# Kernel optimization log

Hardware: AMD Instinct MI355X
Metric: run time of the kernel (lower is better)

The kernel has to match this reference:

```python
import jax, jax.numpy as jnp
import numpy as np

B, T, F, U = 64, 256, 64, 512  # batch, bid_sequence, features, lstm units


def setup_inputs() -> dict:
    key = jax.random.key(0)
    ks = jax.random.split(key, 8)
    sc = 0.05
    return {
        "inputs": jax.random.normal(ks[0], (B, T, F), jnp.float32),
        "kernel": jax.random.normal(ks[1], (F, 4 * U), jnp.float32) * sc,      # LSTM input kernel (i,f,c,o)
        "rec_kernel": jax.random.normal(ks[2], (U, 4 * U), jnp.float32) * sc,  # LSTM recurrent kernel
        "bias": jax.random.normal(ks[3], (4 * U,), jnp.float32) * sc,          # LSTM bias
        "att_W": jax.random.normal(ks[4], (T, T), jnp.float32) * sc,           # row t = weights of attention_denses[t] (first t cols used)
        "att_b": jax.random.normal(ks[5], (T,), jnp.float32) * sc,             # bias of attention_denses[t]
        "out_W": jax.random.normal(ks[6], (U,), jnp.float32) * sc,             # final Dense(1) kernel
        "out_b": jax.random.normal(ks[7], (), jnp.float32) * sc,               # final Dense(1) bias
    }


def reference(inputs, kernel, rec_kernel, bias, att_W, att_b, out_W, out_b):
    Bs, Ts, _ = inputs.shape
    Us = rec_kernel.shape[0]

    # ---- LSTM (keras LSTMCell, gate order i,f,c,o; sigmoid/tanh) ----
    xz = jnp.einsum('btf,fg->btg', inputs, kernel) + bias  # precompute input projection

    def step(carry, z):
        h, c = carry
        g = z + h @ rec_kernel
        i, f, gc, o = jnp.split(g, 4, axis=-1)
        c = jax.nn.sigmoid(f) * c + jax.nn.sigmoid(i) * jnp.tanh(gc)
        h = jax.nn.sigmoid(o) * jnp.tanh(c)
        return (h, c), h

    init = (jnp.zeros((Bs, Us), inputs.dtype), jnp.zeros((Bs, Us), inputs.dtype))
    _, hs = jax.lax.scan(step, init, jnp.swapaxes(xz, 0, 1))
    x = jnp.swapaxes(hs, 0, 1)  # (B, T, U)

    # ---- attention_loop ----
    # keras Attention([x[:t], [x[t]]]) softmaxes over a single key -> weights are
    # exactly 1, so attn output is x[t] tiled t times; transpose + Dense_t(1)
    # collapses to sum(att_W[t, :t]) * x[t] + att_b[t]. Step 0 passes x[0] through.
    t_idx = jnp.arange(Ts)
    tri = (t_idx[None, :] < t_idx[:, None]).astype(x.dtype)  # row t: first t cols valid
    coef = jnp.where(t_idx == 0, jnp.asarray(1.0, x.dtype), jnp.sum(att_W * tri, axis=1))
    shift = jnp.where(t_idx == 0, jnp.asarray(0.0, x.dtype), att_b)
    att = x * coef[None, :, None] + shift[None, :, None]  # (B, T, U)

    # ---- final Dense(1) + reshape + sigmoid ----
    return jax.nn.sigmoid(jnp.einsum('btu,u->bt', att, out_W) + out_b)  # (B, T)
```

## Files before the change

kernel.cpp:

```cpp
#include <hip/hip_runtime.h>
#include <hip/hip_bf16.h>
#include <string.h>

#define B_ 64
#define T_ 256
#define F_ 64
#define U_ 512
#define G4_ 2048
#define KTOT 576
#define KSTEPS 18

typedef __attribute__((ext_vector_type(8))) short short8;
typedef __attribute__((ext_vector_type(4))) float v4f;
typedef __attribute__((ext_vector_type(4))) int i4;
typedef unsigned short u16;

__device__ __forceinline__ float bf2f(u16 b) {
    unsigned int x = ((unsigned int)b) << 16;
    float f; memcpy(&f, &x, 4); return f;
}
__device__ __forceinline__ u16 f2bf(float f) {
    __hip_bfloat16 h = __float2bfloat16(f);
    u16 b; memcpy(&b, &h, 2); return b;
}
__device__ __forceinline__ float sigmoidf_(float x) { return 1.f / (1.f + __expf(-x)); }
__device__ __forceinline__ float tanhf_(float x) {
    float xc = fminf(15.f, fmaxf(-15.f, x));
    float e = __expf(2.f * xc);
    return (e - 1.f) / (e + 1.f);
}

__device__ __forceinline__ float ldany(const void* p, size_t i, int fg) {
    return fg ? ((const float*)p)[i] : bf2f(((const u16*)p)[i]);
}

#define WS_FLAG   0
#define WS_XB     64
#define WS_WP     2097216
#define WS_H2     4456512
#define WS_DOT    4718656
#define WS_BIASF  4784192
#define WS_ATTWF  4792384
#define WS_ATTBF  5054528
#define WS_OUTWF  5055552
#define WS_OUTBF  5057600
#define WS_NEED   5057920

__global__ __launch_bounds__(256) void detect(const unsigned int* __restrict__ w,
                                              int* __restrict__ flag) {
    __shared__ int votes;
    if (threadIdx.x == 0) votes = 0;
    __syncthreads();
    unsigned int v = w[threadIdx.x];
    int e = (v >> 7) & 0xFF;
    if (e >= 100 && e <= 135) atomicAdd(&votes, 1);
    __syncthreads();
    if (threadIdx.x == 0) *flag = (votes < 200) ? 1 : 0;
}

__global__ __launch_bounds__(256) void convert(const void* __restrict__ x,
                                               const void* __restrict__ bias,
                                               const void* __restrict__ attW,
                                               const void* __restrict__ attb,
                                               const void* __restrict__ outW,
                                               const void* __restrict__ outb,
                                               const int* __restrict__ flag,
                                               u16* __restrict__ xb,
                                               float* __restrict__ biasf,
                                               float* __restrict__ attWf,
                                               float* __restrict__ attbf,
                                               float* __restrict__ outWf,
                                               float* __restrict__ outbf,
                                               float* __restrict__ dot,
                                               unsigned int* __restrict__ h2z) {
    int fg = *flag;
    size_t i = (size_t)blockIdx.x * 256 + threadIdx.x;
    if (i < 1048576) {
        float v = ldany(x, i, fg);
        int b = (int)(i >> 14), t = (int)((i >> 6) & 255), f = (int)(i & 63);
        xb[((size_t)t * B_ + b) * F_ + f] = f2bf(v);
        return;
    }
    i -= 1048576;
    if (i < 2048)  { biasf[i] = ldany(bias, i, fg); return; }
    i -= 2048;
    if (i < 65536) { attWf[i] = ldany(attW, i, fg); return; }
    i -= 65536;
    if (i < 256)   { attbf[i] = ldany(attb, i, fg); return; }
    i -= 256;
    if (i < 512)   { outWf[i] = ldany(outW, i, fg); return; }
    i -= 512;
    if (i < 1)     { outbf[i] = ldany(outb, i, fg); return; }
    i -= 1;
    if (i < 16384) { dot[i] = 0.f; return; }
    i -= 16384;
    if (i < 32768) { h2z[i] = 0u; return; }
}

__global__ __launch_bounds__(256) void pack_w(const void* __restrict__ kin,
                                              const void* __restrict__ krec,
                                              const int* __restrict__ flag,
                                              u16* __restrict__ Wp) {
    int fg = *flag;
    int gid = blockIdx.x * 256 + threadIdx.x;
    int lane = gid & 63;
    int frag = gid >> 6;
    int nt = frag / KSTEPS;
    int ks = frag - nt * KSTEPS;
    int kbase = ks * 32 + (lane >> 4) * 8;
    int cp = nt * 16 + (lane & 15);
    int u = cp >> 2, gate = cp & 3;
    int C = gate * U_ + u;
    short8 v;
    for (int j = 0; j < 8; j++) {
        int k = kbase + j;
        float w = (k < F_) ? ldany(kin, (size_t)k * G4_ + C, fg)
                           : ldany(krec, (size_t)(k - F_) * G4_ + C, fg);
        v[j] = (short)f2bf(w);
    }
    *reinterpret_cast<short8*>(Wp + (size_t)gid * 8) = v;
}

__global__ __launch_bounds__(512, 2) void lstm_persist(const u16* __restrict__ xb,
                                                       const float* __restrict__ biasf,
                                                       const float* __restrict__ outWf,
                                                       const u16* __restrict__ Wp,
                                                       u16* __restrict__ h2,
                                                       float* __restrict__ dot) {
    __shared__ __align__(16) u16 stage[16 * 520];
    __shared__ __align__(16) float gbuf[16][164];
    __shared__ float dp[32][16];

    int tid = threadIdx.x;
    int bid = blockIdx.x;
    int rg = bid & 3;
    int gu = bid >> 2;
    int w = tid >> 6, l = tid & 63;
    int nt = gu * 8 + w;

    short8 W[KSTEPS];
    #pragma unroll
    for (int ks = 0; ks < KSTEPS; ks++)
        W[ks] = *reinterpret_cast<const short8*>(Wp + ((size_t)(nt * KSTEPS + ks) * 64 + l) * 8);

    int arow = rg * 16 + (l & 15);
    int koff = (l >> 4) * 8;
    int plr = 2 * w + (l >> 5);
    int pcol = (l & 31) * 16;
    int er = tid >> 5;
    int ui = tid & 31;
    int unit = gu * 32 + ui;
    float bia = biasf[0 * U_ + unit], bif = biasf[1 * U_ + unit];
    float big = biasf[2 * U_ + unit], bio = biasf[3 * U_ + unit];
    float wout = outWf[unit];
    float c = 0.f;

    for (int t = 0; t < T_; t++) {
        u16* hcur = h2 + (size_t)(t & 1) * (B_ * U_);
        const u16* hprev = h2 + (size_t)((t + 1) & 1) * (B_ * U_);
        unsigned int wtag = ((unsigned)(t >> 1) & 1u) ^ 1u;
        unsigned int rpat = ((((unsigned)(t - 1) >> 1) & 1u) ^ 1u) * 0x00010001u;

        i4 q0, q1;
        {
            const void* bp = (const void*)(hprev + (size_t)(rg * 16 + plr) * U_ + pcol);
            int spins = 0;
            for (;;) {
                asm volatile(
                    "global_load_dwordx4 %0, %2, off sc0 sc1\n\t"
                    "global_load_dwordx4 %1, %2, off offset:16 sc0 sc1\n\t"
                    "s_waitcnt vmcnt(0)"
                    : "=v"(q0), "=v"(q1) : "v"(bp) : "memory");
                if (t == 0) break;
                unsigned bad = 0;
                bad |= (((unsigned)q0[0]) ^ rpat) & 0x00010001u;
                bad |= (((unsigned)q0[1]) ^ rpat) & 0x00010001u;
                bad |= (((unsigned)q0[2]) ^ rpat) & 0x00010001u;
                bad |= (((unsigned)q0[3]) ^ rpat) & 0x00010001u;
                bad |= (((unsigned)q1[0]) ^ rpat) & 0x00010001u;
                bad |= (((unsigned)q1[1]) ^ rpat) & 0x00010001u;
                bad |= (((unsigned)q1[2]) ^ rpat) & 0x00010001u;
                bad |= (((unsigned)q1[3]) ^ rpat) & 0x00010001u;
                if (__ballot(bad == 0) == ~0ull) break;
                if (++spins > (1 << 14)) break;
                __builtin_amdgcn_s_sleep(2);
            }
        }
        *reinterpret_cast<i4*>(&stage[plr * 520 + pcol])     = q0;
        *reinterpret_cast<i4*>(&stage[plr * 520 + pcol + 8]) = q1;
        __syncthreads();

        const u16* xrow = xb + ((size_t)t * B_ + arow) * F_;
        short8 a0 = *reinterpret_cast<const short8*>(xrow + koff);
        short8 a1 = *reinterpret_cast<const short8*>(xrow + 32 + koff);
        v4f acc0 = {0.f, 0.f, 0.f, 0.f}, acc1 = {0.f, 0.f, 0.f, 0.f};
        acc0 = __builtin_amdgcn_mfma_f32_16x16x32_bf16(a0, W[0], acc0, 0, 0, 0);
        acc1 = __builtin_amdgcn_mfma_f32_16x16x32_bf16(a1, W[1], acc1, 0, 0, 0);
        #pragma unroll
        for (int ks = 2; ks < KSTEPS; ks += 2) {
            short8 ah0 = *reinterpret_cast<const short8*>(
                &stage[(l & 15) * 520 + (ks - 2) * 32 + koff]);
            short8 ah1 = *reinterpret_cast<const short8*>(
                &stage[(l & 15) * 520 + (ks - 1) * 32 + koff]);
            acc0 = __builtin_amdgcn_mfma_f32_16x16x32_bf16(ah0, W[ks],     acc0, 0, 0, 0);
            acc1 = __builtin_amdgcn_mfma_f32_16x16x32_bf16(ah1, W[ks + 1], acc1, 0, 0, 0);
        }
        v4f acc = acc0 + acc1;

        {
            int c0 = 16 * w + (l & 15);
            int coff = 5 * (c0 >> 2) + (c0 & 3);
            int rb = (l >> 4) * 4;
            #pragma unroll
            for (int rr = 0; rr < 4; rr++)
                gbuf[rb + rr][coff] = acc[rr];
        }
        __syncthreads();

        {
            const float* gr = &gbuf[er][5 * ui];
            float ig = sigmoidf_(gr[0] + bia);
            float fg = sigmoidf_(gr[1] + bif);
            float gc = tanhf_(gr[2] + big);
            float og = sigmoidf_(gr[3] + bio);
            c = fg * c + ig * gc;
            float h = og * tanhf_(c);

            float hp = __shfl_xor(h, 1, 64);
            if ((ui & 1) == 0) {
                unsigned int pk = (unsigned int)(((unsigned)f2bf(h)  & 0xFFFEu) | wtag)
                                | ((unsigned int)(((unsigned)f2bf(hp) & 0xFFFEu) | wtag) << 16);
                void* sp = (void*)(hcur + (size_t)(rg * 16 + er) * U_ + unit);
                asm volatile("global_store_dword %0, %1, off sc0 sc1"
                             :: "v"(sp), "v"(pk) : "memory");
            }

            float s = h * wout;
            s += __shfl_xor(s, 1, 64);
            s += __shfl_xor(s, 2, 64);
            s += __shfl_xor(s, 4, 64);
            s += __shfl_xor(s, 8, 64);
            s += __shfl_xor(s, 16, 64);
            if (ui == 0) dp[t & 31][er] = s;
        }

        if ((t & 31) == 31) {
            __syncthreads();
            int t0 = t - 31;
            int tt = tid >> 4, row = tid & 15;
            atomicAdd(&dot[(size_t)(rg * 16 + row) * T_ + (t0 + tt)], dp[tt][row]);
        }
    }
}

__global__ __launch_bounds__(256) void finale(const float* __restrict__ attWf,
                                              const float* __restrict__ attbf,
                                              const float* __restrict__ outWf,
                                              const float* __restrict__ outbf,
                                              const float* __restrict__ dot,
                                              const int* __restrict__ flag,
                                              void* __restrict__ out) {
    __shared__ float red[256];
    int t = blockIdx.x, tid = threadIdx.x;
    int fg = *flag;

    float v = (tid < t) ? attWf[(size_t)t * T_ + tid] : 0.f;
    red[tid] = v; __syncthreads();
    for (int s = 128; s > 0; s >>= 1) { if (tid < s) red[tid] += red[tid + s]; __syncthreads(); }
    float coef = (t == 0) ? 1.f : red[0];
    __syncthreads();
    red[tid] = outWf[tid] + outWf[tid + 256]; __syncthreads();
    for (int s = 128; s > 0; s >>= 1) { if (tid < s) red[tid] += red[tid + s]; __syncthreads(); }
    float sumW = red[0];

    float base = ((t == 0) ? 0.f : attbf[t]) * sumW + outbf[0];

    if (tid < B_) {
        float s = sigmoidf_(coef * dot[(size_t)tid * T_ + t] + base);
        size_t idx = (size_t)tid * T_ + t;
        if (fg) ((float*)out)[idx] = s;
        else    ((u16*)out)[idx] = f2bf(s);
    }
}

extern "C" void kernel_launch(void* const* d_in, const int* in_sizes, int n_in,
                              void* d_out, int out_size, void* d_ws, size_t ws_size,
                              hipStream_t stream) {
    const void* x    = d_in[0];
    const void* kin  = d_in[1];
    const void* krec = d_in[2];
    const void* bias = d_in[3];
    const void* attW = d_in[4];
    const void* attb = d_in[5];
    const void* outW = d_in[6];
    const void* outb = d_in[7];

    if (ws_size < (size_t)WS_NEED) return;

    char* ws = (char*)d_ws;
    int*   flag  = (int*)(ws + WS_FLAG);
    u16*   xb    = (u16*)(ws + WS_XB);
    u16*   Wp    = (u16*)(ws + WS_WP);
    u16*   h2    = (u16*)(ws + WS_H2);
    float* dot   = (float*)(ws + WS_DOT);
    float* biasf = (float*)(ws + WS_BIASF);
    float* attWf = (float*)(ws + WS_ATTWF);
    float* attbf = (float*)(ws + WS_ATTBF);
    float* outWf = (float*)(ws + WS_OUTWF);
    float* outbf = (float*)(ws + WS_OUTBF);

    detect<<<1, 256, 0, stream>>>((const unsigned int*)kin, flag);
    convert<<<4556, 256, 0, stream>>>(x, bias, attW, attb, outW, outb, flag,
                                      xb, biasf, attWf, attbf, outWf, outbf, dot,
                                      (unsigned int*)h2);
    pack_w<<<576, 256, 0, stream>>>(kin, krec, flag, Wp);
    lstm_persist<<<64, 512, 0, stream>>>(xb, biasf, outWf, Wp, h2, dot);
    finale<<<256, 256, 0, stream>>>(attWf, attbf, outWf, outbf, dot, flag, d_out);
}
```

Baseline: 684.7 us.

## Repartition persistent LSTM blocks to 8 batch rows by 64 units

```diff
diff --git a/kernel.cpp b/kernel.cpp
--- a/kernel.cpp
+++ b/kernel.cpp
@@ -127,33 +127,36 @@
                                                        const u16* __restrict__ Wp,
                                                        u16* __restrict__ h2,
                                                        float* __restrict__ dot) {
-    __shared__ __align__(16) u16 stage[16 * 520];
-    __shared__ __align__(16) float gbuf[16][164];
-    __shared__ float dp[32][16];
+    __shared__ __align__(16) u16 stage[8 * 520];
+    __shared__ __align__(16) float gbuf[8][324];
+    __shared__ float dp[32][8];
 
     int tid = threadIdx.x;
     int bid = blockIdx.x;
-    int rg = bid & 3;
-    int gu = bid >> 2;
+    int rg = bid & 7;
+    int gu = bid >> 3;
     int w = tid >> 6, l = tid & 63;
-    int nt = gu * 8 + w;
-
-    short8 W[KSTEPS];
+
+    int nt0 = gu * 16 + 2 * w;
+    short8 W0[KSTEPS], W1[KSTEPS];
     #pragma unroll
-    for (int ks = 0; ks < KSTEPS; ks++)
-        W[ks] = *reinterpret_cast<const short8*>(Wp + ((size_t)(nt * KSTEPS + ks) * 64 + l) * 8);
-
-    int arow = rg * 16 + (l & 15);
+    for (int ks = 0; ks < KSTEPS; ks++) {
+        W0[ks] = *reinterpret_cast<const short8*>(Wp + ((size_t)(nt0 * KSTEPS + ks) * 64 + l) * 8);
+        W1[ks] = *reinterpret_cast<const short8*>(Wp + ((size_t)((nt0 + 1) * KSTEPS + ks) * 64 + l) * 8);
+    }
+
+    int lrow = (l & 15) & 7;
+    int arow = rg * 8 + lrow;
     int koff = (l >> 4) * 8;
-    int plr = 2 * w + (l >> 5);
-    int pcol = (l & 31) * 16;
-    int er = tid >> 5;
-    int ui = tid & 31;
-    int unit = gu * 32 + ui;
+    int sbase = lrow * 520 + koff;
+    int er = w;
+    int ui = l;
+    int unit = gu * 64 + ui;
     float bia = biasf[0 * U_ + unit], bif = biasf[1 * U_ + unit];
     float big = biasf[2 * U_ + unit], bio = biasf[3 * U_ + unit];
     float wout = outWf[unit];
     float c = 0.f;
+    int fm = 1;
 
     for (int t = 0; t < T_; t++) {
         u16* hcur = h2 + (size_t)(t & 1) * (B_ * U_);
@@ -161,59 +164,70 @@
         unsigned int wtag = ((unsigned)(t >> 1) & 1u) ^ 1u;
         unsigned int rpat = ((((unsigned)(t - 1) >> 1) & 1u) ^ 1u) * 0x00010001u;
 
-        i4 q0, q1;
+        i4 q0;
         {
-            const void* bp = (const void*)(hprev + (size_t)(rg * 16 + plr) * U_ + pcol);
+            const void* bp = (const void*)(hprev + (size_t)(rg * 8 + w) * U_ + l * 8);
             int spins = 0;
             for (;;) {
-                asm volatile(
-                    "global_load_dwordx4 %0, %2, off sc0 sc1\n\t"
-                    "global_load_dwordx4 %1, %2, off offset:16 sc0 sc1\n\t"
-                    "s_waitcnt vmcnt(0)"
-                    : "=v"(q0), "=v"(q1) : "v"(bp) : "memory");
+                if (fm)
+                    asm volatile(
+                        "global_load_dwordx4 %0, %1, off sc0\n\t"
+                        "s_waitcnt vmcnt(0)"
+                        : "=v"(q0) : "v"(bp) : "memory");
+                else
+                    asm volatile(
+                        "global_load_dwordx4 %0, %1, off sc0 sc1\n\t"
+                        "s_waitcnt vmcnt(0)"
+                        : "=v"(q0) : "v"(bp) : "memory");
                 if (t == 0) break;
                 unsigned bad = 0;
                 bad |= (((unsigned)q0[0]) ^ rpat) & 0x00010001u;
                 bad |= (((unsigned)q0[1]) ^ rpat) & 0x00010001u;
                 bad |= (((unsigned)q0[2]) ^ rpat) & 0x00010001u;
                 bad |= (((unsigned)q0[3]) ^ rpat) & 0x00010001u;
-                bad |= (((unsigned)q1[0]) ^ rpat) & 0x00010001u;
-                bad |= (((unsigned)q1[1]) ^ rpat) & 0x00010001u;
-                bad |= (((unsigned)q1[2]) ^ rpat) & 0x00010001u;
-                bad |= (((unsigned)q1[3]) ^ rpat) & 0x00010001u;
                 if (__ballot(bad == 0) == ~0ull) break;
-                if (++spins > (1 << 14)) break;
+                if (++spins == 512) fm = 0;
+                if (spins > (1 << 14)) break;
                 __builtin_amdgcn_s_sleep(2);
             }
         }
-        *reinterpret_cast<i4*>(&stage[plr * 520 + pcol])     = q0;
-        *reinterpret_cast<i4*>(&stage[plr * 520 + pcol + 8]) = q1;
+        *reinterpret_cast<i4*>(&stage[w * 520 + l * 8]) = q0;
         __syncthreads();
 
         const u16* xrow = xb + ((size_t)t * B_ + arow) * F_;
         short8 a0 = *reinterpret_cast<const short8*>(xrow + koff);
         short8 a1 = *reinterpret_cast<const short8*>(xrow + 32 + koff);
-        v4f acc0 = {0.f, 0.f, 0.f, 0.f}, acc1 = {0.f, 0.f, 0.f, 0.f};
-        acc0 = __builtin_amdgcn_mfma_f32_16x16x32_bf16(a0, W[0], acc0, 0, 0, 0);
-        acc1 = __builtin_amdgcn_mfma_f32_16x16x32_bf16(a1, W[1], acc1, 0, 0, 0);
+        v4f acc00 = {0.f, 0.f, 0.f, 0.f}, acc01 = {0.f, 0.f, 0.f, 0.f};
+        v4f acc10 = {0.f, 0.f, 0.f, 0.f}, acc11 = {0.f, 0.f, 0.f, 0.f};
+        acc00 = __builtin_amdgcn_mfma_f32_16x16x32_bf16(a0, W0[0], acc00, 0, 0, 0);
+        acc01 = __builtin_amdgcn_mfma_f32_16x16x32_bf16(a1, W0[1], acc01, 0, 0, 0);
+        acc10 = __builtin_amdgcn_mfma_f32_16x16x32_bf16(a0, W1[0], acc10, 0, 0, 0);
+        acc11 = __builtin_amdgcn_mfma_f32_16x16x32_bf16(a1, W1[1], acc11, 0, 0, 0);
         #pragma unroll
         for (int ks = 2; ks < KSTEPS; ks += 2) {
-            short8 ah0 = *reinterpret_cast<const short8*>(
-                &stage[(l & 15) * 520 + (ks - 2) * 32 + koff]);
-            short8 ah1 = *reinterpret_cast<const short8*>(
-                &stage[(l & 15) * 520 + (ks - 1) * 32 + koff]);
-            acc0 = __builtin_amdgcn_mfma_f32_16x16x32_bf16(ah0, W[ks],     acc0, 0, 0, 0);
-            acc1 = __builtin_amdgcn_mfma_f32_16x16x32_bf16(ah1, W[ks + 1], acc1, 0, 0, 0);
-        }
-        v4f acc = acc0 + acc1;
+            short8 ah0 = *reinterpret_cast<const short8*>(&stage[sbase + (ks - 2) * 32]);
+            short8 ah1 = *reinterpret_cast<const short8*>(&stage[sbase + (ks - 1) * 32]);
+            acc00 = __builtin_amdgcn_mfma_f32_16x16x32_bf16(ah0, W0[ks],     acc00, 0, 0, 0);
+            acc01 = __builtin_amdgcn_mfma_f32_16x16x32_bf16(ah1, W0[ks + 1], acc01, 0, 0, 0);
+            acc10 = __builtin_amdgcn_mfma_f32_16x16x32_bf16(ah0, W1[ks],     acc10, 0, 0, 0);
+            acc11 = __builtin_amdgcn_mfma_f32_16x16x32_bf16(ah1, W1[ks + 1], acc11, 0, 0, 0);
+        }
+        v4f accA = acc00 + acc01;
+        v4f accB = acc10 + acc11;
 
         {
-            int c0 = 16 * w + (l & 15);
-            int coff = 5 * (c0 >> 2) + (c0 & 3);
             int rb = (l >> 4) * 4;
-            #pragma unroll
-            for (int rr = 0; rr < 4; rr++)
-                gbuf[rb + rr][coff] = acc[rr];
+            if (rb < 8) {
+                int cA = 16 * (2 * w) + (l & 15);
+                int cB = cA + 16;
+                int coA = 5 * (cA >> 2) + (cA & 3);
+                int coB = 5 * (cB >> 2) + (cB & 3);
+                #pragma unroll
+                for (int rr = 0; rr < 4; rr++) {
+                    gbuf[rb + rr][coA] = accA[rr];
+                    gbuf[rb + rr][coB] = accB[rr];
+                }
+            }
         }
         __syncthreads();
 
@@ -230,7 +244,7 @@
             if ((ui & 1) == 0) {
                 unsigned int pk = (unsigned int)(((unsigned)f2bf(h)  & 0xFFFEu) | wtag)
                                 | ((unsigned int)(((unsigned)f2bf(hp) & 0xFFFEu) | wtag) << 16);
-                void* sp = (void*)(hcur + (size_t)(rg * 16 + er) * U_ + unit);
+                void* sp = (void*)(hcur + (size_t)(rg * 8 + er) * U_ + unit);
                 asm volatile("global_store_dword %0, %1, off sc0 sc1"
                              :: "v"(sp), "v"(pk) : "memory");
             }
@@ -241,14 +255,17 @@
             s += __shfl_xor(s, 4, 64);
             s += __shfl_xor(s, 8, 64);
             s += __shfl_xor(s, 16, 64);
+            s += __shfl_xor(s, 32, 64);
             if (ui == 0) dp[t & 31][er] = s;
         }
 
         if ((t & 31) == 31) {
             __syncthreads();
             int t0 = t - 31;
-            int tt = tid >> 4, row = tid & 15;
-            atomicAdd(&dot[(size_t)(rg * 16 + row) * T_ + (t0 + tt)], dp[tt][row]);
+            if (tid < 256) {
+                int tt = tid >> 3, row = tid & 7;
+                atomicAdd(&dot[(size_t)(rg * 8 + row) * T_ + (t0 + tt)], dp[tt][row]);
+            }
         }
     }
 }
```

New measurement: 959.6 us. 1.4x slower.

## Replace LDS gate transpose with in-register shuffles and hoist input MFMAs before spin-wait

Applied to the files above, without the earlier changes.

```diff
diff --git a/kernel.cpp b/kernel.cpp
--- a/kernel.cpp
+++ b/kernel.cpp
@@ -121,15 +121,14 @@
     *reinterpret_cast<short8*>(Wp + (size_t)gid * 8) = v;
 }
 
-__global__ __launch_bounds__(512, 2) void lstm_persist(const u16* __restrict__ xb,
+__global__ __launch_bounds__(512, 1) void lstm_persist(const u16* __restrict__ xb,
                                                        const float* __restrict__ biasf,
                                                        const float* __restrict__ outWf,
                                                        const u16* __restrict__ Wp,
                                                        u16* __restrict__ h2,
                                                        float* __restrict__ dot) {
     __shared__ __align__(16) u16 stage[16 * 520];
-    __shared__ __align__(16) float gbuf[16][164];
-    __shared__ float dp[32][16];
+    __shared__ float dp[32][16][9];
 
     int tid = threadIdx.x;
     int bid = blockIdx.x;
@@ -147,9 +146,10 @@
     int koff = (l >> 4) * 8;
     int plr = 2 * w + (l >> 5);
     int pcol = (l & 31) * 16;
-    int er = tid >> 5;
-    int ui = tid & 31;
-    int unit = gu * 32 + ui;
+    int e = l & 3;
+    int j = (l >> 2) & 3;
+    int erow = 4 * (l >> 4) + e;
+    int unit = 4 * nt + j;
     float bia = biasf[0 * U_ + unit], bif = biasf[1 * U_ + unit];
     float big = biasf[2 * U_ + unit], bio = biasf[3 * U_ + unit];
     float wout = outWf[unit];
@@ -160,6 +160,14 @@
         const u16* hprev = h2 + (size_t)((t + 1) & 1) * (B_ * U_);
         unsigned int wtag = ((unsigned)(t >> 1) & 1u) ^ 1u;
         unsigned int rpat = ((((unsigned)(t - 1) >> 1) & 1u) ^ 1u) * 0x00010001u;
+
+        const u16* xrow = xb + ((size_t)t * B_ + arow) * F_;
+        short8 a0 = *reinterpret_cast<const short8*>(xrow + koff);
+        short8 a1 = *reinterpret_cast<const short8*>(xrow + 32 + koff);
+        v4f acc0 = {0.f, 0.f, 0.f, 0.f}, acc1 = {0.f, 0.f, 0.f, 0.f};
+        acc0 = __builtin_amdgcn_mfma_f32_16x16x32_bf16(a0, W[0], acc0, 0, 0, 0);
+        acc1 = __builtin_amdgcn_mfma_f32_16x16x32_bf16(a1, W[1], acc1, 0, 0, 0);
+        __builtin_amdgcn_sched_barrier(0);
 
         i4 q0, q1;
         {
@@ -190,12 +198,6 @@
         *reinterpret_cast<i4*>(&stage[plr * 520 + pcol + 8]) = q1;
         __syncthreads();
 
-        const u16* xrow = xb + ((size_t)t * B_ + arow) * F_;
-        short8 a0 = *reinterpret_cast<const short8*>(xrow + koff);
-        short8 a1 = *reinterpret_cast<const short8*>(xrow + 32 + koff);
-        v4f acc0 = {0.f, 0.f, 0.f, 0.f}, acc1 = {0.f, 0.f, 0.f, 0.f};
-        acc0 = __builtin_amdgcn_mfma_f32_16x16x32_bf16(a0, W[0], acc0, 0, 0, 0);
-        acc1 = __builtin_amdgcn_mfma_f32_16x16x32_bf16(a1, W[1], acc1, 0, 0, 0);
         #pragma unroll
         for (int ks = 2; ks < KSTEPS; ks += 2) {
             short8 ah0 = *reinterpret_cast<const short8*>(
@@ -207,48 +209,57 @@
         }
         v4f acc = acc0 + acc1;
 
+        float g0 = acc[0], g1 = acc[1], g2 = acc[2], g3 = acc[3];
         {
-            int c0 = 16 * w + (l & 15);
-            int coff = 5 * (c0 >> 2) + (c0 & 3);
-            int rb = (l >> 4) * 4;
-            #pragma unroll
-            for (int rr = 0; rr < 4; rr++)
-                gbuf[rb + rr][coff] = acc[rr];
-        }
-        __syncthreads();
+            float t0 = __shfl_xor(g1, 1, 64);
+            float t1 = __shfl_xor(g0, 1, 64);
+            float t2 = __shfl_xor(g3, 1, 64);
+            float t3 = __shfl_xor(g2, 1, 64);
+            float b0 = ((0 ^ e) & 1) ? t0 : g0;
+            float b1 = ((1 ^ e) & 1) ? t1 : g1;
+            float b2 = ((2 ^ e) & 1) ? t2 : g2;
+            float b3 = ((3 ^ e) & 1) ? t3 : g3;
+            float u0 = __shfl_xor(b2, 2, 64);
+            float u1 = __shfl_xor(b3, 2, 64);
+            float u2 = __shfl_xor(b0, 2, 64);
+            float u3 = __shfl_xor(b1, 2, 64);
+            g0 = ((0 ^ e) & 2) ? u0 : b0;
+            g1 = ((1 ^ e) & 2) ? u1 : b1;
+            g2 = ((2 ^ e) & 2) ? u2 : b2;
+            g3 = ((3 ^ e) & 2) ? u3 : b3;
+        }
 
         {
-            const float* gr = &gbuf[er][5 * ui];
-            float ig = sigmoidf_(gr[0] + bia);
-            float fg = sigmoidf_(gr[1] + bif);
-            float gc = tanhf_(gr[2] + big);
-            float og = sigmoidf_(gr[3] + bio);
+            float ig = sigmoidf_(g0 + bia);
+            float fg = sigmoidf_(g1 + bif);
+            float gc = tanhf_(g2 + big);
+            float og = sigmoidf_(g3 + bio);
             c = fg * c + ig * gc;
             float h = og * tanhf_(c);
 
-            float hp = __shfl_xor(h, 1, 64);
-            if ((ui & 1) == 0) {
+            float hp = __shfl_xor(h, 4, 64);
+            if (((l >> 2) & 1) == 0) {
                 unsigned int pk = (unsigned int)(((unsigned)f2bf(h)  & 0xFFFEu) | wtag)
                                 | ((unsigned int)(((unsigned)f2bf(hp) & 0xFFFEu) | wtag) << 16);
-                void* sp = (void*)(hcur + (size_t)(rg * 16 + er) * U_ + unit);
+                void* sp = (void*)(hcur + (size_t)(rg * 16 + erow) * U_ + unit);
                 asm volatile("global_store_dword %0, %1, off sc0 sc1"
                              :: "v"(sp), "v"(pk) : "memory");
             }
 
             float s = h * wout;
-            s += __shfl_xor(s, 1, 64);
-            s += __shfl_xor(s, 2, 64);
             s += __shfl_xor(s, 4, 64);
             s += __shfl_xor(s, 8, 64);
-            s += __shfl_xor(s, 16, 64);
-            if (ui == 0) dp[t & 31][er] = s;
+            if ((l & 12) == 0) dp[t & 31][erow][w] = s;
         }
 
         if ((t & 31) == 31) {
             __syncthreads();
-            int t0 = t - 31;
+            int t0_ = t - 31;
             int tt = tid >> 4, row = tid & 15;
-            atomicAdd(&dot[(size_t)(rg * 16 + row) * T_ + (t0 + tt)], dp[tt][row]);
+            float sum = 0.f;
+            #pragma unroll
+            for (int ww = 0; ww < 8; ww++) sum += dp[tt][row][ww];
+            atomicAdd(&dot[(size_t)(rg * 16 + row) * T_ + (t0_ + tt)], sum);
         }
     }
 }
```

After: 608.9 us (median of 2 runs). 1.12x faster.
